# Optimization experiments

Hardware: AMD Instinct MI355X
Metric: run time of the kernel (lower is better)

## Reference

```python
import jax, jax.numpy as jnp
import numpy as np

N = 50000
E = 800000
F_IN = 1433
H = 256
C = 7


def setup_inputs() -> dict:
    key = jax.random.key(0)
    ks = jax.random.split(key, 8)
    x = jax.random.normal(ks[0], (N, F_IN), dtype=jnp.float32)
    edge_index = jax.random.randint(ks[1], (2, E), 0, N, dtype=jnp.int32)
    # glorot init for linear weights
    def glorot(k, fan_in, fan_out):
        s = jnp.sqrt(6.0 / (fan_in + fan_out)).astype(jnp.float32)
        return jax.random.uniform(k, (fan_in, fan_out), jnp.float32, -s, s)
    W1 = glorot(ks[2], F_IN, H)
    W2 = glorot(ks[3], H, H)
    W3 = glorot(ks[4], H, C)
    b1 = jnp.zeros((H,), jnp.float32)
    b2 = jnp.zeros((H,), jnp.float32)
    b3 = jnp.zeros((C,), jnp.float32)
    return {"x": x, "edge_index": edge_index, "W1": W1, "b1": b1,
            "W2": W2, "b2": b2, "W3": W3, "b3": b3}


def _gcn_norm(edge_index, num_nodes):
    # add self-loops, edge_weight = 1, symmetric normalization
    row = jnp.concatenate([edge_index[0], jnp.arange(num_nodes, dtype=edge_index.dtype)])
    col = jnp.concatenate([edge_index[1], jnp.arange(num_nodes, dtype=edge_index.dtype)])
    w = jnp.ones(row.shape[0], dtype=jnp.float32)
    deg = jax.ops.segment_sum(w, col, num_segments=num_nodes)  # degree on target (col)
    dinv = jnp.where(deg > 0, jax.lax.rsqrt(deg), 0.0)
    norm = dinv[row] * dinv[col]  # [E+N]
    return row, col, norm


def _gcn_layer(x, W, b, row, col, norm, num_nodes):
    h = x @ W                                   # [N, F_out]
    msg = h[row] * norm[:, None]                # gather + scale, [E+N, F_out]
    out = jax.ops.segment_sum(msg, col, num_segments=num_nodes)  # scatter-add
    return out + b


def reference(x, edge_index, W1, b1, W2, b2, W3, b3):
    row, col, norm = _gcn_norm(edge_index, N)
    h = jax.nn.relu(_gcn_layer(x, W1, b1, row, col, norm, N))
    h = jax.nn.relu(_gcn_layer(h, W2, b2, row, col, norm, N))
    h = _gcn_layer(h, W3, b3, row, col, norm, N)
    return jax.nn.log_softmax(h, axis=1)
```

## Files before the change

### kernel.cpp

```cpp
#include <hip/hip_runtime.h>
#include <math.h>

#define NNODES 50000
#define NEDGES 800000
#define FIN    1433
#define KP1    1472
#define HDIM   256
#define NCLS   7
#define MPAD   50048
#define G1B    782

typedef __attribute__((ext_vector_type(8))) short short8;
typedef __attribute__((ext_vector_type(4))) float f32x4;

__device__ __forceinline__ unsigned short f2bf(float f) {
    unsigned u = __builtin_bit_cast(unsigned, f);
    u += 0x7fffu + ((u >> 16) & 1u);
    return (unsigned short)(u >> 16);
}

__device__ __forceinline__ float bf2f(unsigned short u) {
    unsigned v = ((unsigned)u) << 16;
    return __builtin_bit_cast(float, v);
}

__device__ __forceinline__ void gl2lds16(const void* g, void* l) {
    __builtin_amdgcn_global_load_lds(
        (const __attribute__((address_space(1))) unsigned int*)g,
        (__attribute__((address_space(3))) unsigned int*)l, 16, 0, 0);
}

__device__ __forceinline__ f32x4 ld4u(const float* p) {
    f32x4 v; __builtin_memcpy(&v, p, 16); return v;
}


#define NB_COUNT 3125
#define NB_CAST  1728

__global__ void count_cast(const int* __restrict__ col, int* __restrict__ cnt,
                           const float* __restrict__ W1, const float* __restrict__ W2,
                           unsigned short* __restrict__ w1t, unsigned short* __restrict__ w2t) {
    int b = blockIdx.x;
    if (b < NB_COUNT) {
        int e = b * 256 + threadIdx.x;
        if (e < NEDGES) atomicAdd(&cnt[col[e]], 1);
    } else {
        int idx = (b - NB_COUNT) * 256 + threadIdx.x;
        if (idx < HDIM * KP1) {
            int n = idx / KP1, k = idx % KP1;
            w1t[idx] = f2bf((k < FIN) ? W1[(size_t)k * HDIM + n] : 0.f);
        } else {
            int j = idx - HDIM * KP1;
            if (j < HDIM * HDIM) {
                int n = j / HDIM, k = j % HDIM;
                w2t[j] = f2bf(W2[(size_t)k * HDIM + n]);
            }
        }
    }
}

#define SCAN_BS 512
#define NSB     98

__global__ __launch_bounds__(SCAN_BS) void scan_part(const int* __restrict__ cnt,
                                                     int* __restrict__ bsum, int n) {
    __shared__ int red[SCAN_BS];
    int t = threadIdx.x;
    int i = blockIdx.x * SCAN_BS + t;
    red[t] = (i < n) ? cnt[i] : 0;
    __syncthreads();
    for (int off = SCAN_BS / 2; off > 0; off >>= 1) {
        if (t < off) red[t] += red[t + off];
        __syncthreads();
    }
    if (t == 0) bsum[blockIdx.x] = red[0];
}

__global__ __launch_bounds__(SCAN_BS) void scan_apply(const int* __restrict__ cnt,
                                                      const int* __restrict__ bsum,
                                                      int* __restrict__ rp,
                                                      float* __restrict__ dinv,
                                                      int n, int total) {
    __shared__ int s[SCAN_BS];
    __shared__ int bs[128];
    __shared__ int base;
    int t = threadIdx.x;
    if (t < 128) bs[t] = (t < NSB) ? bsum[t] : 0;
    int i = blockIdx.x * SCAN_BS + t;
    int v = (i < n) ? cnt[i] : 0;
    s[t] = v;
    __syncthreads();
    if (t == 0) {
        int acc = 0;
        for (int j = 0; j < blockIdx.x; ++j) acc += bs[j];
        base = acc;
    }
    for (int off = 1; off < SCAN_BS; off <<= 1) {
        int u = (t >= off) ? s[t - off] : 0;
        __syncthreads();
        s[t] += u;
        __syncthreads();
    }
    if (i < n) {
        rp[i] = base + s[t] - v;
        dinv[i] = rsqrtf((float)(v + 1));
    }
    if (i == n) rp[n] = total;
}


__global__ __launch_bounds__(256) void fill_gemm1(const float* __restrict__ X,
                                                  const unsigned short* __restrict__ Bt,
                                                  unsigned short* __restrict__ C,
                                                  const int* __restrict__ row,
                                                  const int* __restrict__ col,
                                                  const int* __restrict__ rp,
                                                  int* __restrict__ cur,
                                                  int2* __restrict__ csrw,
                                                  const float* __restrict__ dinv) {
    __shared__ __align__(16) unsigned short As[64 * 64];
    __shared__ __align__(16) unsigned short Bs[256 * 64];

    if (blockIdx.x >= G1B) {
        int e = (blockIdx.x - G1B) * 256 + threadIdx.x;
        if (e < NEDGES) {
            int c = col[e], r = row[e];
            int pos = rp[c] + atomicAdd(&cur[c], 1);
            csrw[pos] = make_int2(r, __float_as_int(dinv[r] * dinv[c]));
        }
        return;
    }

    const int tid = threadIdx.x;
    const int wave = tid >> 6, lane = tid & 63;
    const int m0 = blockIdx.x * 64;
    const int wn = wave * 64;
    const int kq = lane >> 4, l16 = lane & 15;
    const int lq = lane >> 4;
    const int h  = lane & 15;

    int rowbase[4];
    #pragma unroll
    for (int i = 0; i < 4; ++i) {
        int r = m0 + wave * 16 + i * 4 + lq;
        if (r >= NNODES) r = NNODES - 1;
        rowbase[i] = r * FIN;
    }
    int aw[4];
    #pragma unroll
    for (int i = 0; i < 4; ++i) {
        int r7 = lq + 4 * (i & 1);
        aw[i] = (wave * 16 + i * 4 + lq) * 64 + (((h >> 1) ^ r7) * 8) + (h & 1) * 4;
    }

    int bo[8];
    #pragma unroll
    for (int i = 0; i < 8; ++i) {
        int c = i * 256 + tid;
        int n = c >> 3, ccg = (c & 7) ^ (n & 7);
        bo[i] = n * KP1 + ccg * 8;
    }

    int aoffb[2], boffb[2];
    #pragma unroll
    for (int ks = 0; ks < 2; ++ks) {
        int swz = ((ks * 4 + kq) ^ (l16 & 7)) * 8;
        aoffb[ks] = l16 * 64 + swz;
        boffb[ks] = (wn + l16) * 64 + swz;
    }

    f32x4 acc[4][4] = {};
    constexpr int NT = KP1 / 64;

    f32x4 fv[4];
    #pragma unroll
    for (int i = 0; i < 4; ++i) fv[i] = ld4u(&X[rowbase[i] + h * 4]);

    for (int t = 0; t < NT; ++t) {
        const int k0 = t * 64;
        #pragma unroll
        for (int i = 0; i < 8; ++i)
            gl2lds16(Bt + bo[i] + k0, &Bs[(i * 256 + tid) * 8]);
        #pragma unroll
        for (int i = 0; i < 4; ++i) {
            ushort4 pk = make_ushort4(f2bf(fv[i].x), f2bf(fv[i].y),
                                      f2bf(fv[i].z), f2bf(fv[i].w));
            *(ushort4*)&As[aw[i]] = pk;
        }
        __syncthreads();

        f32x4 nv[4];
        const bool more = (t + 1 < NT);
        if (more) {
            const int kb = k0 + 64 + h * 4;
            if (t + 2 == NT) {
                #pragma unroll
                for (int i = 0; i < 4; ++i) {
                    float a = (kb + 0 < FIN) ? X[rowbase[i] + kb + 0] : 0.f;
                    float b = (kb + 1 < FIN) ? X[rowbase[i] + kb + 1] : 0.f;
                    float c = (kb + 2 < FIN) ? X[rowbase[i] + kb + 2] : 0.f;
                    float d = (kb + 3 < FIN) ? X[rowbase[i] + kb + 3] : 0.f;
                    nv[i] = (f32x4){a, b, c, d};
                }
            } else {
                #pragma unroll
                for (int i = 0; i < 4; ++i) nv[i] = ld4u(&X[rowbase[i] + kb]);
            }
        }

        #pragma unroll
        for (int ks = 0; ks < 2; ++ks) {
            short8 af[4], bg[4];
            #pragma unroll
            for (int i = 0; i < 4; ++i) af[i] = *(const short8*)&As[i * 1024 + aoffb[ks]];
            #pragma unroll
            for (int j = 0; j < 4; ++j) bg[j] = *(const short8*)&Bs[j * 1024 + boffb[ks]];
            #pragma unroll
            for (int i = 0; i < 4; ++i)
                #pragma unroll
                for (int j = 0; j < 4; ++j)
                    acc[i][j] = __builtin_amdgcn_mfma_f32_16x16x32_bf16(af[i], bg[j], acc[i][j], 0, 0, 0);
        }
        __syncthreads();
        if (more) {
            #pragma unroll
            for (int i = 0; i < 4; ++i) fv[i] = nv[i];
        }
    }

    #pragma unroll
    for (int i = 0; i < 4; ++i) {
        int gm_base = m0 + i * 16 + (lane >> 4) * 4;
        #pragma unroll
        for (int r = 0; r < 4; ++r) {
            int gm = gm_base + r;
            if (gm < NNODES) {
                #pragma unroll
                for (int j = 0; j < 4; ++j) {
                    int gn = wn + j * 16 + l16;
                    C[(size_t)gm * HDIM + gn] = f2bf(acc[i][j][r]);
                }
            }
        }
    }
}


__global__ __launch_bounds__(256) void gemm2_lds(const unsigned short* __restrict__ A,
                                                 const unsigned short* __restrict__ Bt,
                                                 unsigned short* __restrict__ C) {
    __shared__ __align__(16) unsigned short As[64 * 64];
    __shared__ __align__(16) unsigned short Bs[256 * 64];
    const int tid = threadIdx.x;
    const int wave = tid >> 6, lane = tid & 63;
    const int m0 = blockIdx.x * 64;
    const int wn = wave * 64;
    const int kq = lane >> 4, l16 = lane & 15;

    int ao[2];
    #pragma unroll
    for (int i = 0; i < 2; ++i) {
        int c = i * 256 + tid;
        int m = c >> 3, ccg = (c & 7) ^ (m & 7);
        ao[i] = (m0 + m) * HDIM + ccg * 8;
    }
    int bo[8];
    #pragma unroll
    for (int i = 0; i < 8; ++i) {
        int c = i * 256 + tid;
        int n = c >> 3, ccg = (c & 7) ^ (n & 7);
        bo[i] = n * HDIM + ccg * 8;
    }
    int aoffb[2], boffb[2];
    #pragma unroll
    for (int ks = 0; ks < 2; ++ks) {
        int swz = ((ks * 4 + kq) ^ (l16 & 7)) * 8;
        aoffb[ks] = l16 * 64 + swz;
        boffb[ks] = (wn + l16) * 64 + swz;
    }

    f32x4 acc[4][4] = {};
    #pragma unroll
    for (int k0 = 0; k0 < HDIM; k0 += 64) {
        #pragma unroll
        for (int i = 0; i < 2; ++i) gl2lds16(A + ao[i] + k0, &As[(i * 256 + tid) * 8]);
        #pragma unroll
        for (int i = 0; i < 8; ++i) gl2lds16(Bt + bo[i] + k0, &Bs[(i * 256 + tid) * 8]);
        __syncthreads();
        #pragma unroll
        for (int ks = 0; ks < 2; ++ks) {
            short8 af[4], bg[4];
            #pragma unroll
            for (int i = 0; i < 4; ++i) af[i] = *(const short8*)&As[i * 1024 + aoffb[ks]];
            #pragma unroll
            for (int j = 0; j < 4; ++j) bg[j] = *(const short8*)&Bs[j * 1024 + boffb[ks]];
            #pragma unroll
            for (int i = 0; i < 4; ++i)
                #pragma unroll
                for (int j = 0; j < 4; ++j)
                    acc[i][j] = __builtin_amdgcn_mfma_f32_16x16x32_bf16(af[i], bg[j], acc[i][j], 0, 0, 0);
        }
        __syncthreads();
    }

    #pragma unroll
    for (int i = 0; i < 4; ++i) {
        int gm_base = m0 + i * 16 + (lane >> 4) * 4;
        #pragma unroll
        for (int r = 0; r < 4; ++r) {
            int gm = gm_base + r;
            if (gm < NNODES) {
                #pragma unroll
                for (int j = 0; j < 4; ++j) {
                    int gn = wn + j * 16 + l16;
                    C[(size_t)gm * HDIM + gn] = f2bf(acc[i][j][r]);
                }
            }
        }
    }
}


__device__ __forceinline__ void aggregate_row(const ushort4* __restrict__ h, int lane,
                                              int p, int p1,
                                              const int2* __restrict__ csrw,
                                              float& ax, float& ay, float& az, float& aw) {
    for (; p + 8 <= p1; p += 8) {
        int2 e[8];
        #pragma unroll
        for (int j = 0; j < 8; ++j) e[j] = csrw[p + j];
        ushort4 t[8];
        #pragma unroll
        for (int j = 0; j < 8; ++j) t[j] = h[e[j].x * 64 + lane];
        #pragma unroll
        for (int j = 0; j < 8; ++j) {
            float w = __int_as_float(e[j].y);
            ax += w * bf2f(t[j].x); ay += w * bf2f(t[j].y);
            az += w * bf2f(t[j].z); aw += w * bf2f(t[j].w);
        }
    }
    if (p + 4 <= p1) {
        int2 e[4];
        #pragma unroll
        for (int j = 0; j < 4; ++j) e[j] = csrw[p + j];
        ushort4 t[4];
        #pragma unroll
        for (int j = 0; j < 4; ++j) t[j] = h[e[j].x * 64 + lane];
        #pragma unroll
        for (int j = 0; j < 4; ++j) {
            float w = __int_as_float(e[j].y);
            ax += w * bf2f(t[j].x); ay += w * bf2f(t[j].y);
            az += w * bf2f(t[j].z); aw += w * bf2f(t[j].w);
        }
        p += 4;
    }
    for (; p < p1; ++p) {
        int2 e = csrw[p];
        float w = __int_as_float(e.y);
        ushort4 t = h[e.x * 64 + lane];
        ax += w * bf2f(t.x); ay += w * bf2f(t.y); az += w * bf2f(t.z); aw += w * bf2f(t.w);
    }
}


__global__ __launch_bounds__(256) void agg_kernel(const ushort4* __restrict__ h,
                                                  ushort4* __restrict__ out,
                                                  const float* __restrict__ dinv,
                                                  const int* __restrict__ rp,
                                                  const int2* __restrict__ csrw,
                                                  const float* __restrict__ bias,
                                                  int n) {
    int node = blockIdx.x * 4 + (threadIdx.x >> 6);
    int lane = threadIdx.x & 63;
    if (node >= n) return;
    float di = dinv[node];
    float sw = di * di;
    ushort4 hv = h[node * 64 + lane];
    float ax = sw * bf2f(hv.x), ay = sw * bf2f(hv.y);
    float az = sw * bf2f(hv.z), aw = sw * bf2f(hv.w);
    aggregate_row(h, lane, rp[node], rp[node + 1], csrw, ax, ay, az, aw);
    float4 b = ((const float4*)bias)[lane];
    ax = fmaxf(ax + b.x, 0.f); ay = fmaxf(ay + b.y, 0.f);
    az = fmaxf(az + b.z, 0.f); aw = fmaxf(aw + b.w, 0.f);
    out[node * 64 + lane] = make_ushort4(f2bf(ax), f2bf(ay), f2bf(az), f2bf(aw));
}


__global__ __launch_bounds__(256) void agg2_mm3_kernel(const ushort4* __restrict__ h,
                                                       float* __restrict__ h3p,
                                                       const float* __restrict__ dinv,
                                                       const int* __restrict__ rp,
                                                       const int2* __restrict__ csrw,
                                                       const float* __restrict__ bias,
                                                       const float* __restrict__ W3,
                                                       int n) {
    __shared__ __align__(16) float Ws[NCLS * HDIM];
    int tid = threadIdx.x;
    for (int i = tid; i < NCLS * HDIM; i += 256)
        Ws[i] = W3[(i & 255) * NCLS + (i >> 8)];
    __syncthreads();

    int node = blockIdx.x * 4 + (tid >> 6);
    int lane = tid & 63;
    if (node >= n) return;
    float di = dinv[node];
    float sw = di * di;
    ushort4 hv = h[node * 64 + lane];
    float ax = sw * bf2f(hv.x), ay = sw * bf2f(hv.y);
    float az = sw * bf2f(hv.z), aw = sw * bf2f(hv.w);
    aggregate_row(h, lane, rp[node], rp[node + 1], csrw, ax, ay, az, aw);
    float4 b = ((const float4*)bias)[lane];
    ax = fmaxf(ax + b.x, 0.f); ay = fmaxf(ay + b.y, 0.f);
    az = fmaxf(az + b.z, 0.f); aw = fmaxf(aw + b.w, 0.f);

    float p7[NCLS];
    #pragma unroll
    for (int c = 0; c < NCLS; ++c) {
        float4 w4 = *(const float4*)&Ws[c * HDIM + 4 * lane];
        p7[c] = ax * w4.x + ay * w4.y + az * w4.z + aw * w4.w;
    }
    #pragma unroll
    for (int c = 0; c < NCLS; ++c)
        for (int off = 32; off > 0; off >>= 1) p7[c] += __shfl_down(p7[c], off);
    if (lane == 0) {
        *(float4*)&h3p[node * 8]     = make_float4(p7[0], p7[1], p7[2], p7[3]);
        *(float4*)&h3p[node * 8 + 4] = make_float4(p7[4], p7[5], p7[6], 0.f);
    }
}


__global__ void final_kernel(const float* __restrict__ h3p, const float* __restrict__ dinv,
                             const int* __restrict__ rp, const int2* __restrict__ csrw,
                             const float* __restrict__ b3, float* __restrict__ out, int n) {
    int i = blockIdx.x * blockDim.x + threadIdx.x;
    if (i >= n) return;
    const float4* H = (const float4*)h3p;
    float di = dinv[i];
    float sw = di * di;
    float4 su = H[i * 2], sv = H[i * 2 + 1];
    float a0 = sw * su.x, a1 = sw * su.y, a2 = sw * su.z, a3 = sw * su.w;
    float a4 = sw * sv.x, a5 = sw * sv.y, a6 = sw * sv.z;
    int p = rp[i], p1 = rp[i + 1];
    for (; p + 4 <= p1; p += 4) {
        int2 e0 = csrw[p], e1 = csrw[p + 1], e2 = csrw[p + 2], e3 = csrw[p + 3];
        float w0 = __int_as_float(e0.y), w1 = __int_as_float(e1.y);
        float w2 = __int_as_float(e2.y), w3 = __int_as_float(e3.y);
        float4 u0 = H[e0.x * 2], v0 = H[e0.x * 2 + 1];
        float4 u1 = H[e1.x * 2], v1 = H[e1.x * 2 + 1];
        float4 u2 = H[e2.x * 2], v2 = H[e2.x * 2 + 1];
        float4 u3 = H[e3.x * 2], v3 = H[e3.x * 2 + 1];
        a0 += w0 * u0.x + w1 * u1.x + w2 * u2.x + w3 * u3.x;
        a1 += w0 * u0.y + w1 * u1.y + w2 * u2.y + w3 * u3.y;
        a2 += w0 * u0.z + w1 * u1.z + w2 * u2.z + w3 * u3.z;
        a3 += w0 * u0.w + w1 * u1.w + w2 * u2.w + w3 * u3.w;
        a4 += w0 * v0.x + w1 * v1.x + w2 * v2.x + w3 * v3.x;
        a5 += w0 * v0.y + w1 * v1.y + w2 * v2.y + w3 * v3.y;
        a6 += w0 * v0.z + w1 * v1.z + w2 * v2.z + w3 * v3.z;
    }
    for (; p < p1; ++p) {
        int2 e = csrw[p];
        float wg = __int_as_float(e.y);
        float4 u = H[e.x * 2], v = H[e.x * 2 + 1];
        a0 += wg * u.x; a1 += wg * u.y; a2 += wg * u.z; a3 += wg * u.w;
        a4 += wg * v.x; a5 += wg * v.y; a6 += wg * v.z;
    }
    float acc[NCLS] = {a0, a1, a2, a3, a4, a5, a6};
    float mx = -1e30f;
    #pragma unroll
    for (int c = 0; c < NCLS; ++c) { acc[c] += b3[c]; mx = fmaxf(mx, acc[c]); }
    float sum = 0.f;
    #pragma unroll
    for (int c = 0; c < NCLS; ++c) sum += expf(acc[c] - mx);
    float lse = mx + logf(sum);
    #pragma unroll
    for (int c = 0; c < NCLS; ++c) out[i * NCLS + c] = acc[c] - lse;
}


extern "C" void kernel_launch(void* const* d_in, const int* in_sizes, int n_in,
                              void* d_out, int out_size, void* d_ws, size_t ws_size,
                              hipStream_t stream) {
    const float* x  = (const float*)d_in[0];
    const int*   ei = (const int*)d_in[1];
    const float* W1 = (const float*)d_in[2];
    const float* b1 = (const float*)d_in[3];
    const float* W2 = (const float*)d_in[4];
    const float* b2 = (const float*)d_in[5];
    const float* W3 = (const float*)d_in[6];
    const float* b3 = (const float*)d_in[7];
    float* out = (float*)d_out;
    const int* row = ei;
    const int* col = ei + NEDGES;

    char* w = (char*)d_ws;
    auto alloc = [&](size_t b) { void* p = (void*)w; w += (b + 255) & ~(size_t)255; return p; };
    int*   cnt  = (int*)alloc(NNODES * 4);
    int*   cur  = (int*)alloc(NNODES * 4);
    int*   rp   = (int*)alloc((NNODES + 1) * 4);
    float* dinv = (float*)alloc(NNODES * 4);
    int*   bsum = (int*)alloc(128 * 4);
    int2*  csrw = (int2*)alloc((size_t)NEDGES * 8);
    unsigned short* w1t  = (unsigned short*)alloc((size_t)HDIM * KP1 * 2);
    unsigned short* w2t  = (unsigned short*)alloc((size_t)HDIM * HDIM * 2);
    unsigned short* h_bf = (unsigned short*)alloc((size_t)MPAD * HDIM * 2);
    unsigned short* a_bf = (unsigned short*)alloc((size_t)MPAD * HDIM * 2);
    float* h3p = (float*)alloc((size_t)NNODES * 8 * 4);

    const size_t cpad = ((size_t)NNODES * 4 + 255) & ~(size_t)255;
    hipMemsetAsync(cnt, 0, cpad + (size_t)NNODES * 4, stream);

    count_cast<<<NB_COUNT + NB_CAST, 256, 0, stream>>>(col, cnt, W1, W2, w1t, w2t);
    scan_part <<<NSB, SCAN_BS, 0, stream>>>(cnt, bsum, NNODES);
    scan_apply<<<NSB, SCAN_BS, 0, stream>>>(cnt, bsum, rp, dinv, NNODES, NEDGES);

    fill_gemm1<<<G1B + NB_COUNT, 256, 0, stream>>>(x, w1t, h_bf, row, col, rp, cur, csrw, dinv);

    agg_kernel<<<(NNODES + 3) / 4, 256, 0, stream>>>((const ushort4*)h_bf, (ushort4*)a_bf,
                                                     dinv, rp, csrw, b1, NNODES);
    gemm2_lds<<<MPAD / 64, 256, 0, stream>>>(a_bf, w2t, h_bf);
    agg2_mm3_kernel<<<(NNODES + 3) / 4, 256, 0, stream>>>((const ushort4*)h_bf, h3p,
                                                          dinv, rp, csrw, b2, W3, NNODES);
    final_kernel<<<(NNODES + 255) / 256, 256, 0, stream>>>(h3p, dinv, rp, csrw, b3, out, NNODES);
}
```

Baseline: 643.2 us.

## Deepen X prefetch to two tiles ahead and use raw barrier in GEMM1

The first GEMM now prefetches X two k-tiles ahead instead of one, holding an extra register buffer so global load latency is hidden across more MFMA work. The end-of-iteration __syncthreads is replaced by a bare s_barrier wrapped in sched_barriers, which avoids the full waitcnt drain that would otherwise stall on the in-flight prefetch loads. Launch bounds now request 4 blocks per SM. The extra registers could limit occupancy or cause spills, and the bare barrier relies on the LDS writes being complete before it.

Result: slower. 750.6 us (+16.7%).

```diff
diff --git a/kernel.cpp b/kernel.cpp
--- a/kernel.cpp
+++ b/kernel.cpp
@@ -110,15 +110,15 @@
 }
 
 
-__global__ __launch_bounds__(256) void fill_gemm1(const float* __restrict__ X,
-                                                  const unsigned short* __restrict__ Bt,
-                                                  unsigned short* __restrict__ C,
-                                                  const int* __restrict__ row,
-                                                  const int* __restrict__ col,
-                                                  const int* __restrict__ rp,
-                                                  int* __restrict__ cur,
-                                                  int2* __restrict__ csrw,
-                                                  const float* __restrict__ dinv) {
+__global__ __launch_bounds__(256, 4) void fill_gemm1(const float* __restrict__ X,
+                                                     const unsigned short* __restrict__ Bt,
+                                                     unsigned short* __restrict__ C,
+                                                     const int* __restrict__ row,
+                                                     const int* __restrict__ col,
+                                                     const int* __restrict__ rp,
+                                                     int* __restrict__ cur,
+                                                     int2* __restrict__ csrw,
+                                                     const float* __restrict__ dinv) {
     __shared__ __align__(16) unsigned short As[64 * 64];
     __shared__ __align__(16) unsigned short Bs[256 * 64];
 
@@ -173,9 +173,11 @@
     f32x4 acc[4][4] = {};
     constexpr int NT = KP1 / 64;
 
-    f32x4 fv[4];
+    f32x4 fv[4], nx[4];
     #pragma unroll
     for (int i = 0; i < 4; ++i) fv[i] = ld4u(&X[rowbase[i] + h * 4]);
+    #pragma unroll
+    for (int i = 0; i < 4; ++i) nx[i] = ld4u(&X[rowbase[i] + 64 + h * 4]);
 
     for (int t = 0; t < NT; ++t) {
         const int k0 = t * 64;
@@ -190,22 +192,22 @@
         }
         __syncthreads();
 
-        f32x4 nv[4];
-        const bool more = (t + 1 < NT);
-        if (more) {
-            const int kb = k0 + 64 + h * 4;
-            if (t + 2 == NT) {
+        f32x4 tmp[4];
+        const bool have2 = (t + 2 < NT);
+        if (have2) {
+            const int kb = (t + 2) * 64 + h * 4;
+            if (t + 2 == NT - 1) {
                 #pragma unroll
                 for (int i = 0; i < 4; ++i) {
                     float a = (kb + 0 < FIN) ? X[rowbase[i] + kb + 0] : 0.f;
                     float b = (kb + 1 < FIN) ? X[rowbase[i] + kb + 1] : 0.f;
                     float c = (kb + 2 < FIN) ? X[rowbase[i] + kb + 2] : 0.f;
                     float d = (kb + 3 < FIN) ? X[rowbase[i] + kb + 3] : 0.f;
-                    nv[i] = (f32x4){a, b, c, d};
+                    tmp[i] = (f32x4){a, b, c, d};
                 }
             } else {
                 #pragma unroll
-                for (int i = 0; i < 4; ++i) nv[i] = ld4u(&X[rowbase[i] + kb]);
+                for (int i = 0; i < 4; ++i) tmp[i] = ld4u(&X[rowbase[i] + kb]);
             }
         }
 
@@ -222,10 +224,18 @@
                 for (int j = 0; j < 4; ++j)
                     acc[i][j] = __builtin_amdgcn_mfma_f32_16x16x32_bf16(af[i], bg[j], acc[i][j], 0, 0, 0);
         }
-        __syncthreads();
-        if (more) {
-            #pragma unroll
-            for (int i = 0; i < 4; ++i) fv[i] = nv[i];
+
+        __builtin_amdgcn_sched_barrier(0);
+        asm volatile("" ::: "memory");
+        __builtin_amdgcn_s_barrier();
+        asm volatile("" ::: "memory");
+        __builtin_amdgcn_sched_barrier(0);
+
+        #pragma unroll
+        for (int i = 0; i < 4; ++i) fv[i] = nx[i];
+        if (have2) {
+            #pragma unroll
+            for (int i = 0; i < 4; ++i) nx[i] = tmp[i];
         }
     }
 
```
